# Kernel optimization log

Hardware: AMD Instinct MI355X
Metric: run time of the kernel (lower is better)

Reference implementation:

```python
import jax, jax.numpy as jnp
import numpy as np

N_HEADS = 16


def _apply_rope(x, rope):
    # x: [B, H, N, Dh], rope: [B, N, Dh]; consecutive (even, odd) pairs form complex numbers
    xr, xi = x[..., 0::2], x[..., 1::2]              # [B,H,N,Dh/2]
    rr, ri = rope[:, None, :, 0::2], rope[:, None, :, 1::2]  # [B,1,N,Dh/2]
    or_ = xr * rr - xi * ri
    oi = xr * ri + xi * rr
    return jnp.stack([or_, oi], axis=-1).reshape(x.shape)


def setup_inputs() -> dict:
    key = jax.random.key(0)
    ks = jax.random.split(key, 8)
    B, N, D, Dh = 2, 2048, 2048, 128
    s = 0.02
    return {
        "x": jax.random.normal(ks[0], (B, N, D), jnp.float32),
        "q_rope": jax.random.normal(ks[1], (B, N, Dh), jnp.float32),
        "k_rope": jax.random.normal(ks[2], (B, N, Dh), jnp.float32),
        "Wq": jax.random.normal(ks[3], (D, D), jnp.float32) * s,
        "Wk": jax.random.normal(ks[4], (D, D), jnp.float32) * s,
        "Wv": jax.random.normal(ks[5], (D, D), jnp.float32) * s,
        "Wo": jax.random.normal(ks[6], (D, D), jnp.float32) * s,
        "bo": jax.random.normal(ks[7], (D,), jnp.float32) * s,
    }


def reference(x, q_rope, k_rope, Wq, Wk, Wv, Wo, bo):
    B, N, D = x.shape
    H = N_HEADS
    Dh = D // H
    # QKV projections (weights stored as [in, out])
    q = (x @ Wq).reshape(B, N, H, Dh).transpose(0, 2, 1, 3)  # [B,H,N,Dh]
    k = (x @ Wk).reshape(B, N, H, Dh).transpose(0, 2, 1, 3)
    v = (x @ Wv).reshape(B, N, H, Dh).transpose(0, 2, 1, 3)
    # NOTE: original scales q by d_head^-0.5 AND F.sdpa applies its default
    # 1/sqrt(d_head) scale again -> total score scale 1/d_head (faithful).
    q = q * (Dh ** -0.5)
    q = _apply_rope(q, q_rope)
    k = _apply_rope(k, k_rope)
    scores = jnp.einsum('bhnd,bhmd->bhnm', q, k) * (Dh ** -0.5)
    attn = jax.nn.softmax(scores, axis=-1)
    out = jnp.einsum('bhnm,bhmd->bhnd', attn, v)  # [B,H,N,Dh]
    out = out.transpose(0, 2, 1, 3).reshape(B, N, D)
    return out @ Wo + bo
```

## Files before the change

### kernel.cpp

```cpp
#include <hip/hip_runtime.h>
#include <hip/hip_bf16.h>
#include <stdint.h>


typedef __attribute__((ext_vector_type(4))) float f32x4;
typedef __attribute__((ext_vector_type(8))) short bf16x8;

__device__ __forceinline__ unsigned short f2bf(float f){
  unsigned u = __builtin_bit_cast(unsigned, f);
  u += 0x7FFFu + ((u >> 16) & 1u);
  return (unsigned short)(u >> 16);
}
__device__ __forceinline__ float bf2f(unsigned short h){
  unsigned u = ((unsigned)h) << 16;
  return __builtin_bit_cast(float, u);
}
__device__ __forceinline__ void gload16(const void* g, void* l){
  __builtin_amdgcn_global_load_lds((const __attribute__((address_space(1))) void*)g,
                                   (__attribute__((address_space(3))) void*)l, 16, 0, 0);
}

__global__ void k_cvt(const float* __restrict__ src, unsigned short* __restrict__ dst, int n4){
  int i = blockIdx.x * 256 + threadIdx.x;
  if (i >= n4) return;
  float4 v = ((const float4*)src)[i];
  unsigned long long pk = (unsigned long long)f2bf(v.x)
    | ((unsigned long long)f2bf(v.y) << 16)
    | ((unsigned long long)f2bf(v.z) << 32)
    | ((unsigned long long)f2bf(v.w) << 48);
  ((unsigned long long*)dst)[i] = pk;
}

__global__ void k_transpose_all(const float* __restrict__ W0, const float* __restrict__ W1,
                                const float* __restrict__ W2, const float* __restrict__ W3,
                                unsigned short* __restrict__ WT){
  const float* W = (blockIdx.z == 0) ? W0 : (blockIdx.z == 1) ? W1 : (blockIdx.z == 2) ? W2 : W3;
  unsigned short* dst = WT + (size_t)blockIdx.z * 4194304;
  __shared__ float tile[64][65];
  int t = threadIdx.x;
  int cc = t & 63, rb = t >> 6;
  int bx = blockIdx.x * 64;
  int by = blockIdx.y * 64;
  #pragma unroll
  for (int i = 0; i < 16; i++){
    int r = rb + i * 4;
    tile[r][cc] = W[(size_t)(by + r) * 2048 + bx + cc];
  }
  __syncthreads();
  #pragma unroll
  for (int i = 0; i < 16; i++){
    int r = rb + i * 4;
    dst[(size_t)(bx + r) * 2048 + by + cc] = f2bf(tile[cc][r]);
  }
}

__global__ __launch_bounds__(256, 3) void k_gemm_qkv(
    const unsigned short* __restrict__ A,
    const unsigned short* __restrict__ Bt,
    unsigned short* __restrict__ Oq,
    unsigned short* __restrict__ Ok,
    unsigned short* __restrict__ Ov,
    const float* __restrict__ ropeq,
    const float* __restrict__ ropek)
{
  const int Kdim = 2048;
  __shared__ unsigned short As[128 * 64];
  __shared__ unsigned short Bs[128 * 64];
  const int tid = threadIdx.x;
  const int w = tid >> 6, l = tid & 63, g = l >> 4, c = l & 15;
  const int i0 = blockIdx.y * 32 + blockIdx.x;
  const int xcd = i0 & 7, r0 = i0 >> 3;
  const int bm = (xcd * 4 + (r0 & 3)) * 128;
  const int bn = (r0 >> 2) * 128;
  const int mw = (w >> 1) * 64, nw = (w & 1) * 64;
  f32x4 acc[4][4] = {};
  const int srow = l >> 3;
  const int sbyte = (((l & 7) ^ srow) << 4);
  const char* Ab = (const char*)A;
  const char* Bb = (const char*)Bt;
  char* AsB = (char*)As; char* BsB = (char*)Bs;

  for (int kt = 0; kt < Kdim; kt += 64){
    __syncthreads();
    #pragma unroll
    for (int j = 0; j < 4; j++){
      int chunk = w * 4 + j;
      int row = chunk * 8 + srow;
      gload16(Ab + ((size_t)(bm + row) * Kdim + kt) * 2 + sbyte, AsB + chunk * 1024);
      gload16(Bb + ((size_t)(bn + row) * Kdim + kt) * 2 + sbyte, BsB + chunk * 1024);
    }
    __syncthreads();
    #pragma unroll
    for (int kk = 0; kk < 2; kk++){
      bf16x8 av[4], bv[4];
      #pragma unroll
      for (int i = 0; i < 4; i++){
        int m = mw + i * 16 + c;
        av[i] = *(const bf16x8*)(AsB + m * 128 + ((kk * 64 + g * 16) ^ ((m & 7) << 4)));
        int n = nw + i * 16 + c;
        bv[i] = *(const bf16x8*)(BsB + n * 128 + ((kk * 64 + g * 16) ^ ((n & 7) << 4)));
      }
      #pragma unroll
      for (int i = 0; i < 4; i++)
        #pragma unroll
        for (int jj = 0; jj < 4; jj++)
          acc[i][jj] = __builtin_amdgcn_mfma_f32_16x16x32_bf16(av[i], bv[jj], acc[i][jj], 0, 0, 0);
    }
  }

  const int matsel = bn >> 11;
  const int hh = (bn >> 7) & 15;
  if (matsel < 2){
    unsigned short* O = matsel ? Ok : Oq;
    const float* rope = matsel ? ropek : ropeq;
    const float scale = matsel ? 1.0f : (1.0f / 128.0f);
    #pragma unroll
    for (int i = 0; i < 4; i++){
      int m0 = bm + mw + i * 16 + g * 4;
      #pragma unroll
      for (int jj = 0; jj < 4; jj++){
        int d = nw + jj * 16 + c;
        int dbase = d & ~1;
        int odd = d & 1;
        #pragma unroll
        for (int r = 0; r < 4; r++){
          int m = m0 + r;
          int b = m >> 11, tok = m & 2047;
          float v = acc[i][jj][r];
          float vp = __shfl_xor(v, 1);
          float2 rv = *(const float2*)(rope + (((size_t)(b * 2048 + tok)) << 7) + dbase);
          float xr = odd ? vp : v;
          float xi = odd ? v : vp;
          float res = odd ? (xr * rv.y + xi * rv.x) : (xr * rv.x - xi * rv.y);
          O[(((size_t)(b * 16 + hh) * 2048 + tok) << 7) + d] = f2bf(res * scale);
        }
      }
    }
  } else {
    #pragma unroll
    for (int i = 0; i < 4; i++){
      int m0 = bm + mw + i * 16 + g * 4;
      int b = m0 >> 11, tok0 = m0 & 2047;
      #pragma unroll
      for (int jj = 0; jj < 4; jj++){
        int d = nw + jj * 16 + c;
        unsigned long long pk = (unsigned long long)f2bf(acc[i][jj][0])
          | ((unsigned long long)f2bf(acc[i][jj][1]) << 16)
          | ((unsigned long long)f2bf(acc[i][jj][2]) << 32)
          | ((unsigned long long)f2bf(acc[i][jj][3]) << 48);
        *(unsigned long long*)(Ov + ((size_t)(b * 16 + hh) * 128 + d) * 2048 + tok0) = pk;
      }
    }
  }
}

__global__ __launch_bounds__(256, 3) void k_gemm_out(
    const unsigned short* __restrict__ A,
    const unsigned short* __restrict__ Bt,
    float* __restrict__ O,
    const float* __restrict__ bias)
{
  const int Kdim = 2048;
  __shared__ unsigned short As[128 * 64];
  __shared__ unsigned short Bs[128 * 64];
  const int tid = threadIdx.x;
  const int w = tid >> 6, l = tid & 63, g = l >> 4, c = l & 15;
  const int i0 = blockIdx.y * 32 + blockIdx.x;
  const int xcd = i0 & 7, r0 = i0 >> 3;
  const int bm = (xcd * 4 + (r0 & 3)) * 128;
  const int bn = (r0 >> 2) * 128;
  const int mw = (w >> 1) * 64, nw = (w & 1) * 64;
  f32x4 acc[4][4] = {};
  const int srow = l >> 3;
  const int sbyte = (((l & 7) ^ srow) << 4);
  const char* Ab = (const char*)A;
  const char* Bb = (const char*)Bt;
  char* AsB = (char*)As; char* BsB = (char*)Bs;

  for (int kt = 0; kt < Kdim; kt += 64){
    __syncthreads();
    #pragma unroll
    for (int j = 0; j < 4; j++){
      int chunk = w * 4 + j;
      int row = chunk * 8 + srow;
      gload16(Ab + ((size_t)(bm + row) * Kdim + kt) * 2 + sbyte, AsB + chunk * 1024);
      gload16(Bb + ((size_t)(bn + row) * Kdim + kt) * 2 + sbyte, BsB + chunk * 1024);
    }
    __syncthreads();
    #pragma unroll
    for (int kk = 0; kk < 2; kk++){
      bf16x8 av[4], bv[4];
      #pragma unroll
      for (int i = 0; i < 4; i++){
        int m = mw + i * 16 + c;
        av[i] = *(const bf16x8*)(AsB + m * 128 + ((kk * 64 + g * 16) ^ ((m & 7) << 4)));
        int n = nw + i * 16 + c;
        bv[i] = *(const bf16x8*)(BsB + n * 128 + ((kk * 64 + g * 16) ^ ((n & 7) << 4)));
      }
      #pragma unroll
      for (int i = 0; i < 4; i++)
        #pragma unroll
        for (int jj = 0; jj < 4; jj++)
          acc[i][jj] = __builtin_amdgcn_mfma_f32_16x16x32_bf16(av[i], bv[jj], acc[i][jj], 0, 0, 0);
    }
  }
  #pragma unroll
  for (int i = 0; i < 4; i++){
    int m0 = bm + mw + i * 16 + g * 4;
    #pragma unroll
    for (int jj = 0; jj < 4; jj++){
      int n = bn + nw + jj * 16 + c;
      float bv2 = bias[n];
      #pragma unroll
      for (int r = 0; r < 4; r++)
        O[(size_t)(m0 + r) * 2048 + n] = acc[i][jj][r] + bv2;
    }
  }
}

__global__ __launch_bounds__(256, 2) void k_attn(
    const unsigned short* __restrict__ Q,
    const unsigned short* __restrict__ Kg,
    const unsigned short* __restrict__ VT,
    unsigned short* __restrict__ Ao)
{
  __shared__ char sh[81920];
  char* PsB = sh + 65536;
  const int tid = threadIdx.x;
  const int w = tid >> 6, l = tid & 63, g = l >> 4, c = l & 15;
  const int i0 = blockIdx.y * 16 + blockIdx.x;
  const int xcd = i0 & 7, kb2 = i0 >> 3;
  const int bh = xcd * 4 + (kb2 >> 4);
  const int qt = kb2 & 15;
  const char* Qb = (const char*)(Q + (((size_t)bh * 2048 + qt * 128) << 7));
  const char* Kb = (const char*)(Kg + ((size_t)bh << 18));
  const char* Vb = (const char*)(VT + ((size_t)bh << 18));
  const int rsub = l >> 4;
  const int byte0 = (l & 15) << 4;
  const int drow = l >> 3;
  const int vbyte = (((l & 7) ^ drow) << 4);

  #pragma unroll
  for (int j = 0; j < 8; j++){
    int chunk = w * 8 + j;
    int row = chunk * 4 + rsub;
    gload16(Qb + (size_t)row * 256 + (byte0 ^ ((row & 7) << 4)), sh + chunk * 1024);
  }
  __syncthreads();
  bf16x8 qa[4][2];
  #pragma unroll
  for (int kk = 0; kk < 4; kk++)
    #pragma unroll
    for (int mf = 0; mf < 2; mf++){
      int q = w * 32 + mf * 16 + c;
      qa[kk][mf] = *(const bf16x8*)(sh + q * 256 + ((kk * 64 + g * 16) ^ ((q & 7) << 4)));
    }
  __syncthreads();

  auto stageKV = [&](int kv, int buf){
    char* Kc = sh + buf * 16384;
    char* Vc = sh + 32768 + buf * 16384;
    #pragma unroll
    for (int j = 0; j < 4; j++){
      int chunk = w * 4 + j;
      int row = chunk * 4 + rsub;
      gload16(Kb + (size_t)(kv * 64 + row) * 256 + (byte0 ^ ((row & 7) << 4)), Kc + chunk * 1024);
    }
    #pragma unroll
    for (int j = 0; j < 4; j++){
      int chunk = w * 4 + j;
      int d = chunk * 8 + drow;
      gload16(Vb + (size_t)d * 4096 + kv * 128 + vbyte, Vc + chunk * 1024);
    }
  };

  f32x4 oacc[2][8] = {};
  float lpart[2][4] = {};

  stageKV(0, 0);
  __syncthreads();

  for (int kv = 0; kv < 32; kv++){
    int cur = kv & 1;
    if (kv < 31) stageKV(kv + 1, cur ^ 1);
    char* Kc = sh + cur * 16384;
    char* Vc = sh + 32768 + cur * 16384;

    f32x4 sacc[2][4] = {};
    __builtin_amdgcn_s_setprio(1);
    #pragma unroll
    for (int kk = 0; kk < 4; kk++){
      bf16x8 kbf[4];
      #pragma unroll
      for (int nf = 0; nf < 4; nf++){
        int kx = nf * 16 + c;
        kbf[nf] = *(const bf16x8*)(Kc + kx * 256 + ((kk * 64 + g * 16) ^ ((kx & 7) << 4)));
      }
      #pragma unroll
      for (int mf = 0; mf < 2; mf++)
        #pragma unroll
        for (int nf = 0; nf < 4; nf++)
          sacc[mf][nf] = __builtin_amdgcn_mfma_f32_16x16x32_bf16(qa[kk][mf], kbf[nf], sacc[mf][nf], 0, 0, 0);
    }
    __builtin_amdgcn_s_setprio(0);

    #pragma unroll
    for (int mf = 0; mf < 2; mf++)
      #pragma unroll
      for (int nf = 0; nf < 4; nf++)
        #pragma unroll
        for (int r = 0; r < 4; r++){
          float pv = __expf(sacc[mf][nf][r]);
          sacc[mf][nf][r] = pv;
          lpart[mf][r] += pv;
        }

    #pragma unroll
    for (int mf = 0; mf < 2; mf++)
      #pragma unroll
      for (int nf = 0; nf < 4; nf++)
        #pragma unroll
        for (int r = 0; r < 4; r++){
          int q = w * 32 + mf * 16 + g * 4 + r;
          int key = nf * 16 + c;
          *(unsigned short*)(PsB + q * 128 + ((key * 2) ^ (((q >> 2) & 3) << 5))) = f2bf(sacc[mf][nf][r]);
        }
    __syncthreads();

    __builtin_amdgcn_s_setprio(1);
    #pragma unroll
    for (int kk = 0; kk < 2; kk++){
      bf16x8 pa[2], vv[8];
      #pragma unroll
      for (int mf = 0; mf < 2; mf++){
        int q = w * 32 + mf * 16 + c;
        pa[mf] = *(const bf16x8*)(PsB + q * 128 + ((kk * 64 + g * 16) ^ (((q >> 2) & 3) << 5)));
      }
      #pragma unroll
      for (int df = 0; df < 8; df++){
        int d = df * 16 + c;
        vv[df] = *(const bf16x8*)(Vc + d * 128 + ((kk * 64 + g * 16) ^ ((d & 7) << 4)));
      }
      #pragma unroll
      for (int mf = 0; mf < 2; mf++)
        #pragma unroll
        for (int df = 0; df < 8; df++)
          oacc[mf][df] = __builtin_amdgcn_mfma_f32_16x16x32_bf16(pa[mf], vv[df], oacc[mf][df], 0, 0, 0);
    }
    __builtin_amdgcn_s_setprio(0);
    __syncthreads();
  }

  int b = bh >> 4, h = bh & 15;
  #pragma unroll
  for (int mf = 0; mf < 2; mf++)
    #pragma unroll
    for (int r = 0; r < 4; r++){
      float s = lpart[mf][r];
      #pragma unroll
      for (int off = 1; off < 16; off <<= 1) s += __shfl_xor(s, off);
      float inv = 1.f / s;
      int qg = qt * 128 + w * 32 + mf * 16 + g * 4 + r;
      size_t rowbase = ((size_t)(b * 2048 + qg)) * 2048 + h * 128;
      #pragma unroll
      for (int df = 0; df < 8; df++)
        Ao[rowbase + df * 16 + c] = f2bf(oacc[mf][df][r] * inv);
    }
}

extern "C" void kernel_launch(void* const* d_in, const int* in_sizes, int n_in,
                              void* d_out, int out_size, void* d_ws, size_t ws_size,
                              hipStream_t stream){
  const float* x      = (const float*)d_in[0];
  const float* q_rope = (const float*)d_in[1];
  const float* k_rope = (const float*)d_in[2];
  const float* Wq     = (const float*)d_in[3];
  const float* Wk     = (const float*)d_in[4];
  const float* Wv     = (const float*)d_in[5];
  const float* Wo     = (const float*)d_in[6];
  const float* bo     = (const float*)d_in[7];
  char* ws = (char*)d_ws;
  unsigned short* xb  = (unsigned short*)(ws);
  unsigned short* wqT = (unsigned short*)(ws + 16777216);
  unsigned short* woT = (unsigned short*)(ws + 41943040);
  unsigned short* qb  = (unsigned short*)(ws + 50331648);
  unsigned short* kbf = (unsigned short*)(ws + 67108864);
  unsigned short* vt  = (unsigned short*)(ws + 83886080);
  unsigned short* ab  = (unsigned short*)(ws + 100663296);

  k_cvt<<<8192, 256, 0, stream>>>(x, xb, 2097152);
  dim3 tg(32, 32, 4);
  k_transpose_all<<<tg, 256, 0, stream>>>(Wq, Wk, Wv, Wo, wqT);
  dim3 gq(32, 48);
  k_gemm_qkv<<<gq, 256, 0, stream>>>(xb, wqT, qb, kbf, vt, q_rope, k_rope);
  dim3 ga(16, 32);
  k_attn<<<ga, 256, 0, stream>>>(qb, kbf, vt, ab);
  dim3 go(32, 16);
  k_gemm_out<<<go, 256, 0, stream>>>(ab, woT, (float*)d_out, bo);
}
```

Measured before the change: 266.8 us.

## Double-buffer GEMM LDS loads with 256x128 tiles and relax attention barrier

```diff
diff --git a/kernel.cpp b/kernel.cpp
--- a/kernel.cpp
+++ b/kernel.cpp
@@ -18,6 +18,10 @@
 __device__ __forceinline__ void gload16(const void* g, void* l){
   __builtin_amdgcn_global_load_lds((const __attribute__((address_space(1))) void*)g,
                                    (__attribute__((address_space(3))) void*)l, 16, 0, 0);
+}
+__device__ __forceinline__ void drain_all(){
+  asm volatile("s_waitcnt vmcnt(0) lgkmcnt(0)" ::: "memory");
+  __builtin_amdgcn_sched_barrier(0);
 }
 
 __global__ void k_cvt(const float* __restrict__ src, unsigned short* __restrict__ dst, int n4){
@@ -54,7 +58,7 @@
   }
 }
 
-__global__ __launch_bounds__(256, 3) void k_gemm_qkv(
+__global__ __launch_bounds__(512, 2) void k_gemm_qkv(
     const unsigned short* __restrict__ A,
     const unsigned short* __restrict__ Bt,
     unsigned short* __restrict__ Oq,
@@ -64,41 +68,54 @@
     const float* __restrict__ ropek)
 {
   const int Kdim = 2048;
-  __shared__ unsigned short As[128 * 64];
-  __shared__ unsigned short Bs[128 * 64];
+  __shared__ char sh[98304];
   const int tid = threadIdx.x;
   const int w = tid >> 6, l = tid & 63, g = l >> 4, c = l & 15;
-  const int i0 = blockIdx.y * 32 + blockIdx.x;
+  const int i0 = blockIdx.y * 16 + blockIdx.x;
   const int xcd = i0 & 7, r0 = i0 >> 3;
-  const int bm = (xcd * 4 + (r0 & 3)) * 128;
-  const int bn = (r0 >> 2) * 128;
+  const int bm = (xcd * 2 + (r0 & 1)) * 256;
+  const int bn = (r0 >> 1) * 128;
   const int mw = (w >> 1) * 64, nw = (w & 1) * 64;
   f32x4 acc[4][4] = {};
   const int srow = l >> 3;
   const int sbyte = (((l & 7) ^ srow) << 4);
   const char* Ab = (const char*)A;
   const char* Bb = (const char*)Bt;
-  char* AsB = (char*)As; char* BsB = (char*)Bs;
-
-  for (int kt = 0; kt < Kdim; kt += 64){
-    __syncthreads();
+
+  auto stage = [&](int kt, int buf){
+    char* Abuf = sh + buf * 49152;
+    char* Bbuf = Abuf + 32768;
     #pragma unroll
     for (int j = 0; j < 4; j++){
-      int chunk = w * 4 + j;
-      int row = chunk * 8 + srow;
-      gload16(Ab + ((size_t)(bm + row) * Kdim + kt) * 2 + sbyte, AsB + chunk * 1024);
-      gload16(Bb + ((size_t)(bn + row) * Kdim + kt) * 2 + sbyte, BsB + chunk * 1024);
-    }
-    __syncthreads();
+      int ch = w * 4 + j;
+      int row = ch * 8 + srow;
+      gload16(Ab + ((size_t)(bm + row) * Kdim + kt) * 2 + sbyte, Abuf + ch * 1024);
+    }
+    #pragma unroll
+    for (int j = 0; j < 2; j++){
+      int ch = w * 2 + j;
+      int row = ch * 8 + srow;
+      gload16(Bb + ((size_t)(bn + row) * Kdim + kt) * 2 + sbyte, Bbuf + ch * 1024);
+    }
+  };
+
+  stage(0, 0);
+  drain_all();
+  __syncthreads();
+  for (int t = 0; t < 32; t++){
+    int cur = t & 1;
+    if (t < 31) stage((t + 1) * 64, cur ^ 1);
+    char* Abuf = sh + cur * 49152;
+    char* Bbuf = Abuf + 32768;
     #pragma unroll
     for (int kk = 0; kk < 2; kk++){
       bf16x8 av[4], bv[4];
       #pragma unroll
       for (int i = 0; i < 4; i++){
         int m = mw + i * 16 + c;
-        av[i] = *(const bf16x8*)(AsB + m * 128 + ((kk * 64 + g * 16) ^ ((m & 7) << 4)));
+        av[i] = *(const bf16x8*)(Abuf + m * 128 + ((kk * 64 + g * 16) ^ ((m & 7) << 4)));
         int n = nw + i * 16 + c;
-        bv[i] = *(const bf16x8*)(BsB + n * 128 + ((kk * 64 + g * 16) ^ ((n & 7) << 4)));
+        bv[i] = *(const bf16x8*)(Bbuf + n * 128 + ((kk * 64 + g * 16) ^ ((n & 7) << 4)));
       }
       #pragma unroll
       for (int i = 0; i < 4; i++)
@@ -106,6 +123,8 @@
         for (int jj = 0; jj < 4; jj++)
           acc[i][jj] = __builtin_amdgcn_mfma_f32_16x16x32_bf16(av[i], bv[jj], acc[i][jj], 0, 0, 0);
     }
+    drain_all();
+    __syncthreads();
   }
 
   const int matsel = bn >> 11;
@@ -154,48 +173,61 @@
   }
 }
 
-__global__ __launch_bounds__(256, 3) void k_gemm_out(
+__global__ __launch_bounds__(512, 2) void k_gemm_out(
     const unsigned short* __restrict__ A,
     const unsigned short* __restrict__ Bt,
     float* __restrict__ O,
     const float* __restrict__ bias)
 {
   const int Kdim = 2048;
-  __shared__ unsigned short As[128 * 64];
-  __shared__ unsigned short Bs[128 * 64];
+  __shared__ char sh[98304];
   const int tid = threadIdx.x;
   const int w = tid >> 6, l = tid & 63, g = l >> 4, c = l & 15;
-  const int i0 = blockIdx.y * 32 + blockIdx.x;
+  const int i0 = blockIdx.y * 16 + blockIdx.x;
   const int xcd = i0 & 7, r0 = i0 >> 3;
-  const int bm = (xcd * 4 + (r0 & 3)) * 128;
-  const int bn = (r0 >> 2) * 128;
+  const int bm = (xcd * 2 + (r0 & 1)) * 256;
+  const int bn = (r0 >> 1) * 128;
   const int mw = (w >> 1) * 64, nw = (w & 1) * 64;
   f32x4 acc[4][4] = {};
   const int srow = l >> 3;
   const int sbyte = (((l & 7) ^ srow) << 4);
   const char* Ab = (const char*)A;
   const char* Bb = (const char*)Bt;
-  char* AsB = (char*)As; char* BsB = (char*)Bs;
-
-  for (int kt = 0; kt < Kdim; kt += 64){
-    __syncthreads();
+
+  auto stage = [&](int kt, int buf){
+    char* Abuf = sh + buf * 49152;
+    char* Bbuf = Abuf + 32768;
     #pragma unroll
     for (int j = 0; j < 4; j++){
-      int chunk = w * 4 + j;
-      int row = chunk * 8 + srow;
-      gload16(Ab + ((size_t)(bm + row) * Kdim + kt) * 2 + sbyte, AsB + chunk * 1024);
-      gload16(Bb + ((size_t)(bn + row) * Kdim + kt) * 2 + sbyte, BsB + chunk * 1024);
-    }
-    __syncthreads();
+      int ch = w * 4 + j;
+      int row = ch * 8 + srow;
+      gload16(Ab + ((size_t)(bm + row) * Kdim + kt) * 2 + sbyte, Abuf + ch * 1024);
+    }
+    #pragma unroll
+    for (int j = 0; j < 2; j++){
+      int ch = w * 2 + j;
+      int row = ch * 8 + srow;
+      gload16(Bb + ((size_t)(bn + row) * Kdim + kt) * 2 + sbyte, Bbuf + ch * 1024);
+    }
+  };
+
+  stage(0, 0);
+  drain_all();
+  __syncthreads();
+  for (int t = 0; t < 32; t++){
+    int cur = t & 1;
+    if (t < 31) stage((t + 1) * 64, cur ^ 1);
+    char* Abuf = sh + cur * 49152;
+    char* Bbuf = Abuf + 32768;
     #pragma unroll
     for (int kk = 0; kk < 2; kk++){
       bf16x8 av[4], bv[4];
       #pragma unroll
       for (int i = 0; i < 4; i++){
         int m = mw + i * 16 + c;
-        av[i] = *(const bf16x8*)(AsB + m * 128 + ((kk * 64 + g * 16) ^ ((m & 7) << 4)));
+        av[i] = *(const bf16x8*)(Abuf + m * 128 + ((kk * 64 + g * 16) ^ ((m & 7) << 4)));
         int n = nw + i * 16 + c;
-        bv[i] = *(const bf16x8*)(BsB + n * 128 + ((kk * 64 + g * 16) ^ ((n & 7) << 4)));
+        bv[i] = *(const bf16x8*)(Bbuf + n * 128 + ((kk * 64 + g * 16) ^ ((n & 7) << 4)));
       }
       #pragma unroll
       for (int i = 0; i < 4; i++)
@@ -203,6 +235,8 @@
         for (int jj = 0; jj < 4; jj++)
           acc[i][jj] = __builtin_amdgcn_mfma_f32_16x16x32_bf16(av[i], bv[jj], acc[i][jj], 0, 0, 0);
     }
+    drain_all();
+    __syncthreads();
   }
   #pragma unroll
   for (int i = 0; i < 4; i++){
@@ -325,7 +359,8 @@
           int key = nf * 16 + c;
           *(unsigned short*)(PsB + q * 128 + ((key * 2) ^ (((q >> 2) & 3) << 5))) = f2bf(sacc[mf][nf][r]);
         }
-    __syncthreads();
+    asm volatile("s_waitcnt lgkmcnt(0)" ::: "memory");
+    __builtin_amdgcn_sched_barrier(0);
 
     __builtin_amdgcn_s_setprio(1);
     #pragma unroll
@@ -348,6 +383,7 @@
           oacc[mf][df] = __builtin_amdgcn_mfma_f32_16x16x32_bf16(pa[mf], vv[df], oacc[mf][df], 0, 0, 0);
     }
     __builtin_amdgcn_s_setprio(0);
+    drain_all();
     __syncthreads();
   }
 
@@ -391,10 +427,10 @@
   k_cvt<<<8192, 256, 0, stream>>>(x, xb, 2097152);
   dim3 tg(32, 32, 4);
   k_transpose_all<<<tg, 256, 0, stream>>>(Wq, Wk, Wv, Wo, wqT);
-  dim3 gq(32, 48);
-  k_gemm_qkv<<<gq, 256, 0, stream>>>(xb, wqT, qb, kbf, vt, q_rope, k_rope);
+  dim3 gq(16, 48);
+  k_gemm_qkv<<<gq, 512, 0, stream>>>(xb, wqT, qb, kbf, vt, q_rope, k_rope);
   dim3 ga(16, 32);
   k_attn<<<ga, 256, 0, stream>>>(qb, kbf, vt, ab);
-  dim3 go(32, 16);
-  k_gemm_out<<<go, 256, 0, stream>>>(ab, woT, (float*)d_out, bo);
-}
+  dim3 go(16, 16);
+  k_gemm_out<<<go, 512, 0, stream>>>(ab, woT, (float*)d_out, bo);
+}
```

After: 255.9 us. 1.04x faster.
